# Optimization experiments

Measured on AMD Instinct MI355X. Metric: run time of the kernel, lower is better.

## Reference

```python
import jax, jax.numpy as jnp
import numpy as np

H, W, BS, CIN = 224, 608, 1, 128
CLS = (16, 12, 10)
PAD = (0, 2, 3)
C12 = CLS[0] * CLS[1]            # 192
C123 = C12 * CLS[2]              # 1920
SUPER = 384
CFACT = C123 // SUPER            # 5
PAD_PROJ = 0.1


def _p(key, shape):
    return jax.random.normal(key, shape, dtype=jnp.float32) * 0.05


def setup_inputs() -> dict:
    key = jax.random.key(0)
    ks = iter(jax.random.split(key, 32))
    d = {"x_in": jax.random.normal(next(ks), (BS, CIN, H, W), dtype=jnp.float32)}
    # stage-1: grouped 1x1 convs (groups=height -> one [out,in] matmul per image line)
    for i, (ci, co) in enumerate([(32, 32), (32, 32), (32, CLS[0] + 2 * PAD[0])]):
        d[f"w1_{i}"] = _p(next(ks), (H, co, ci))
        d[f"b1_{i}"] = _p(next(ks), (H, co))
    # stage-2: CondMul tables indexed by line*16 + stage-1 class
    for i, (ci, co) in enumerate([(32, 32), (32, 32), (32, CLS[1] + 2 * PAD[1])]):
        d[f"w2_{i}"] = _p(next(ks), (H * CLS[0], ci, co))
        d[f"b2_{i}"] = _p(next(ks), (H * CLS[0], co))
    # stage-3: CondMul tables indexed by line*192 + stage-12 class
    for i, (ci, co) in enumerate([(32, 32), (32, 32), (32, CLS[2] + 2 * PAD[2])]):
        d[f"w3_{i}"] = _p(next(ks), (H * C12, ci, co))
        d[f"b3_{i}"] = _p(next(ks), (H * C12, co))
    d["wr0"] = _p(next(ks), (H * SUPER, 32, 32))
    d["br0"] = _p(next(ks), (H * SUPER, 32))
    d["wr1"] = _p(next(ks), (H * C123, 32, 1))
    d["br1"] = _p(next(ks), (H * C123, 1))
    return d


def _condmul(x, inds, w, b):
    # CondMul: y[n] = x[n] @ w[inds[n]] + b[inds[n]]
    return jnp.einsum('ni,nio->no', x, w[inds]) + b[inds]


def _forward(x_in, w1, b1, w2, b2, w3, b3, wr0, br0, wr1, br1):
    bs, _, h, w_ = x_in.shape
    lrelu = jax.nn.leaky_relu  # negative_slope=0.01, same as torch default
    offsets = jnp.arange(h, dtype=jnp.int32).reshape(1, 1, h, 1)
    # ---- stage 1: per-line 1x1 grouped conv stack -> argmax class
    x = x_in[:, 0:32].transpose(0, 2, 1, 3)                    # [b,h,32,w]
    for i in range(3):
        x = jnp.einsum('bhiw,hoi->bhow', x, w1[i]) + b1[i][None, :, :, None]
        if i < 2:
            x = lrelu(x)
    x = x.transpose(0, 2, 1, 3)                                 # [b,16,h,w]
    inds1 = jnp.argmax(x, axis=1)[:, None].astype(jnp.int32)    # [b,1,h,w]
    inds1_l = (inds1 + CLS[0] * offsets).reshape(-1)
    # ---- stage 2: CondMul chain conditioned on (line, class1)
    x = x_in[:, 32:64].transpose(0, 2, 3, 1).reshape(-1, 32)    # [N,32]
    for i in range(3):
        x = _condmul(x, inds1_l, w2[i], b2[i])
        if i < 2:
            x = lrelu(x)
    inds2 = jnp.argmax(x, axis=1).astype(jnp.int32).reshape(bs, 1, h, w_)
    inds12 = inds1 * CLS[1] + (inds2 - PAD[1])
    inds12_l = (jnp.clip(inds12, 0, C12 - 1) + C12 * offsets).reshape(-1)
    # ---- stage 3: CondMul chain conditioned on (line, class12)
    x = x_in[:, 64:96].transpose(0, 2, 3, 1).reshape(-1, 32)
    for i in range(3):
        if i < 2:
            x = lrelu(_condmul(x, inds12_l, w3[i], b3[i]))
        else:
            x = _condmul(x, inds12_l, w3[i], b3[i])
    inds3 = jnp.argmax(x, axis=1).astype(jnp.int32).reshape(bs, 1, h, w_)
    inds123 = jnp.clip(inds12 * CLS[2] + (inds3 - PAD[2]), 0, C123 - 1)
    inds = inds123.reshape(-1)
    lines = jnp.broadcast_to(offsets, (bs, 1, h, w_)).reshape(-1)
    inds_l = inds + C123 * lines                                 # per-leaf index
    inds_super_l = inds // CFACT + SUPER * lines                 # superclass index (reg_line_div=1)
    x = x_in[:, 96:128].transpose(0, 2, 3, 1).reshape(-1, 32)
    x = lrelu(_condmul(x, inds_super_l, wr0, br0))
    r = _condmul(x, inds_l, wr1, br1)[:, 0]                      # [N]
    out = (inds.astype(jnp.float32) + r).reshape(bs, 1, h, w_) / float(C123)
    out = (out - PAD_PROJ) / (1.0 - 2.0 * PAD_PROJ)              # undo projector padding
    return out


def reference(x_in, w1_0, b1_0, w1_1, b1_1, w1_2, b1_2,
              w2_0, b2_0, w2_1, b2_1, w2_2, b2_2,
              w3_0, b3_0, w3_1, b3_1, w3_2, b3_2,
              wr0, br0, wr1, br1):
    return _forward(x_in,
                    (w1_0, w1_1, w1_2), (b1_0, b1_1, b1_2),
                    (w2_0, w2_1, w2_2), (b2_0, b2_1, b2_2),
                    (w3_0, w3_1, w3_2), (b3_0, b3_1, b3_2),
                    wr0, br0, wr1, br1)
```

## Files before the change

### kernel.cpp

```cpp
#include <hip/hip_runtime.h>
#include <cstddef>

#define HH 224
#define WW 608
#define HWSZ (HH * WW)

__device__ __forceinline__ float lrelu(float v) { return v > 0.0f ? v : 0.01f * v; }

template <int CO>
__device__ __forceinline__ void cm4(const float* wmat,
                                    const float* bvec,
                                    int s, const float (&act)[8], float (&acc)[CO / 4]) {
    constexpr int CH = CO / 4;
#pragma unroll
    for (int j = 0; j < CH; j++) acc[j] = 0.0f;
#pragma unroll
    for (int sp = 0; sp < 4; sp++) {
#pragma unroll
        for (int ii = 0; ii < 8; ii++) {
            float xi = __shfl(act[ii], sp, 4);
            const float* wr = wmat + (sp * 8 + ii) * CO + s * CH;
            if constexpr (CH == 8) {
                float4 a = *reinterpret_cast<const float4*>(wr);
                float4 b = *reinterpret_cast<const float4*>(wr + 4);
                acc[0] = fmaf(xi, a.x, acc[0]); acc[1] = fmaf(xi, a.y, acc[1]);
                acc[2] = fmaf(xi, a.z, acc[2]); acc[3] = fmaf(xi, a.w, acc[3]);
                acc[4] = fmaf(xi, b.x, acc[4]); acc[5] = fmaf(xi, b.y, acc[5]);
                acc[6] = fmaf(xi, b.z, acc[6]); acc[7] = fmaf(xi, b.w, acc[7]);
            } else {
                float4 a = *reinterpret_cast<const float4*>(wr);
                acc[0] = fmaf(xi, a.x, acc[0]); acc[1] = fmaf(xi, a.y, acc[1]);
                acc[2] = fmaf(xi, a.z, acc[2]); acc[3] = fmaf(xi, a.w, acc[3]);
            }
        }
    }
#pragma unroll
    for (int j = 0; j < CH; j++) acc[j] += bvec[s * CH + j];
}

__device__ __forceinline__ void wb_lrelu8(float (&act)[8], const float (&acc)[8]) {
#pragma unroll
    for (int j = 0; j < 8; j++) act[j] = lrelu(acc[j]);
}

__device__ __forceinline__ int argmax4(const float (&v)[4], int s) {
    float bv = v[0];
    int bi = 4 * s;
#pragma unroll
    for (int j = 1; j < 4; j++) {
        if (v[j] > bv) { bv = v[j]; bi = 4 * s + j; }
    }
#pragma unroll
    for (int m = 1; m <= 2; m <<= 1) {
        float ov = __shfl_xor(bv, m, 4);
        int oi = __shfl_xor(bi, m, 4);
        if (ov > bv || (ov == bv && oi < bi)) { bv = ov; bi = oi; }
    }
    return bi;
}

template <int NF>
__device__ __forceinline__ void stage_mat(float* ws, const float* __restrict__ src, int lane) {
    const float4* s4 = reinterpret_cast<const float4*>(src);
    float4* w4 = reinterpret_cast<float4*>(ws);
#pragma unroll
    for (int t = 0; t < NF / 4 / 64; t++) w4[t * 64 + lane] = s4[t * 64 + lane];
}

extern "C" __global__ __launch_bounds__(256, 4)
void regressor_fused(const float* __restrict__ x_in,
                     const float* __restrict__ w1_0, const float* __restrict__ b1_0,
                     const float* __restrict__ w1_1, const float* __restrict__ b1_1,
                     const float* __restrict__ w1_2, const float* __restrict__ b1_2,
                     const float* __restrict__ w2_0, const float* __restrict__ b2_0,
                     const float* __restrict__ w2_1, const float* __restrict__ b2_1,
                     const float* __restrict__ w2_2, const float* __restrict__ b2_2,
                     const float* __restrict__ w3_0, const float* __restrict__ b3_0,
                     const float* __restrict__ w3_1, const float* __restrict__ b3_1,
                     const float* __restrict__ w3_2, const float* __restrict__ b3_2,
                     const float* __restrict__ wr0, const float* __restrict__ br0,
                     const float* __restrict__ wr1, const float* __restrict__ br1,
                     float* __restrict__ out) {
    const int h = blockIdx.y;
    const int tid = threadIdx.x;
    const int p = tid >> 2;
    const int s = tid & 3;
    const int lane = tid & 63;
    const int w = blockIdx.x * 64 + p;
    const bool valid = (w < WW);
    const int wc = valid ? w : (WW - 1);
    const int base = h * WW + wc;

    __shared__ __align__(16) float sW0[1024];
    __shared__ __align__(16) float sW1[1024];
    __shared__ __align__(16) float sW2[512];
    __shared__ __align__(16) float sUni[4][1024];
    __shared__ __align__(16) float xbuf[32][65];
    __shared__ int skey[64];
    __shared__ int sperm[64];
    __shared__ int sraw[64];
    __shared__ int sraw2[64];
    float* ws = sUni[tid >> 6];

    for (int tt = tid; tt < 1024; tt += 256) {
        int i = tt >> 5, o = tt & 31;
        sW0[tt] = w1_0[h * 1024 + o * 32 + i];
        sW1[tt] = w1_1[h * 1024 + o * 32 + i];
    }
    for (int tt = tid; tt < 512; tt += 256) {
        int i = tt >> 4, o = tt & 15;
        sW2[tt] = w1_2[h * 512 + o * 32 + i];
    }
    __syncthreads();

    float act[8], acc8[8], acc4[4];

#pragma unroll
    for (int ii = 0; ii < 8; ii++) act[ii] = x_in[(8 * s + ii) * HWSZ + base];
    cm4<32>(sW0, b1_0 + h * 32, s, act, acc8);
    wb_lrelu8(act, acc8);
    cm4<32>(sW1, b1_1 + h * 32, s, act, acc8);
    wb_lrelu8(act, acc8);
    cm4<16>(sW2, b1_2 + h * 16, s, act, acc4);
    const int i1 = argmax4(acc4, s);
    if (s == 0) skey[p] = i1;

#pragma unroll
    for (int ii = 0; ii < 8; ii++)
        xbuf[8 * s + ii][p] = x_in[(32 + 8 * s + ii) * HWSZ + base];
    __syncthreads();
    if (tid < 64) {
        int k = skey[tid], rank = 0;
        for (int j = 0; j < 64; j++) {
            int kj = skey[j];
            rank += (kj < k || (kj == k && j < tid)) ? 1 : 0;
        }
        sperm[rank] = tid;
    }
    __syncthreads();

    {
        const int q = sperm[p];
        const int i1q = skey[q];
#pragma unroll
        for (int ii = 0; ii < 8; ii++) act[ii] = xbuf[8 * s + ii][q];
        const int fc = __builtin_amdgcn_readfirstlane(i1q);
        if (__all(i1q == fc)) {
            const size_t u = (size_t)h * 16 + (size_t)fc;
            stage_mat<1024>(ws, w2_0 + u * 1024, lane);
            cm4<32>(ws, b2_0 + u * 32, s, act, acc8);
            wb_lrelu8(act, acc8);
            stage_mat<1024>(ws, w2_1 + u * 1024, lane);
            cm4<32>(ws, b2_1 + u * 32, s, act, acc8);
            wb_lrelu8(act, acc8);
            stage_mat<512>(ws, w2_2 + u * 512, lane);
            cm4<16>(ws, b2_2 + u * 16, s, act, acc4);
        } else {
            const size_t idx2 = (size_t)h * 16 + (size_t)i1q;
            cm4<32>(w2_0 + idx2 * 1024, b2_0 + idx2 * 32, s, act, acc8);
            wb_lrelu8(act, acc8);
            cm4<32>(w2_1 + idx2 * 1024, b2_1 + idx2 * 32, s, act, acc8);
            wb_lrelu8(act, acc8);
            cm4<16>(w2_2 + idx2 * 512, b2_2 + idx2 * 16, s, act, acc4);
        }
        const int i2 = argmax4(acc4, s);
        if (s == 0) sraw[q] = i1q * 12 + (i2 - 2);
    }
    __syncthreads();

#pragma unroll
    for (int ii = 0; ii < 8; ii++)
        xbuf[8 * s + ii][p] = x_in[(64 + 8 * s + ii) * HWSZ + base];
    if (s == 0) skey[p] = min(max(sraw[p], 0), 191);
    __syncthreads();
    if (tid < 64) {
        int k = skey[tid], rank = 0;
        for (int j = 0; j < 64; j++) {
            int kj = skey[j];
            rank += (kj < k || (kj == k && j < tid)) ? 1 : 0;
        }
        sperm[rank] = tid;
    }
    __syncthreads();

    {
        const int q = sperm[p];
        const int r12 = sraw[q];
        const int c12 = min(max(r12, 0), 191);
#pragma unroll
        for (int ii = 0; ii < 8; ii++) act[ii] = xbuf[8 * s + ii][q];
        const int fc = __builtin_amdgcn_readfirstlane(c12);
        if (__all(c12 == fc)) {
            const size_t u = (size_t)h * 192 + (size_t)fc;
            stage_mat<1024>(ws, w3_0 + u * 1024, lane);
            cm4<32>(ws, b3_0 + u * 32, s, act, acc8);
            wb_lrelu8(act, acc8);
            stage_mat<1024>(ws, w3_1 + u * 1024, lane);
            cm4<32>(ws, b3_1 + u * 32, s, act, acc8);
            wb_lrelu8(act, acc8);
            stage_mat<512>(ws, w3_2 + u * 512, lane);
            cm4<16>(ws, b3_2 + u * 16, s, act, acc4);
        } else {
            const size_t idx3 = (size_t)h * 192 + (size_t)c12;
            cm4<32>(w3_0 + idx3 * 1024, b3_0 + idx3 * 32, s, act, acc8);
            wb_lrelu8(act, acc8);
            cm4<32>(w3_1 + idx3 * 1024, b3_1 + idx3 * 32, s, act, acc8);
            wb_lrelu8(act, acc8);
            cm4<16>(w3_2 + idx3 * 512, b3_2 + idx3 * 16, s, act, acc4);
        }
        const int i3 = argmax4(acc4, s);
        if (s == 0) sraw2[q] = min(max(r12 * 10 + (i3 - 3), 0), 1919);
    }
    __syncthreads();

#pragma unroll
    for (int ii = 0; ii < 8; ii++)
        xbuf[8 * s + ii][p] = x_in[(96 + 8 * s + ii) * HWSZ + base];
    if (s == 0) skey[p] = sraw2[p] / 5;
    __syncthreads();
    if (tid < 64) {
        int k = skey[tid], rank = 0;
        for (int j = 0; j < 64; j++) {
            int kj = skey[j];
            rank += (kj < k || (kj == k && j < tid)) ? 1 : 0;
        }
        sperm[rank] = tid;
    }
    __syncthreads();

    {
        const int q = sperm[p];
        const int leaf = sraw2[q];
        const int sup = leaf / 5;
#pragma unroll
        for (int ii = 0; ii < 8; ii++) act[ii] = xbuf[8 * s + ii][q];
        const int fc = __builtin_amdgcn_readfirstlane(sup);
        if (__all(sup == fc)) {
            const size_t u = (size_t)h * 384 + (size_t)fc;
            stage_mat<1024>(ws, wr0 + u * 1024, lane);
            cm4<32>(ws, br0 + u * 32, s, act, acc8);
        } else {
            const size_t idxs = (size_t)h * 384 + (size_t)sup;
            cm4<32>(wr0 + idxs * 1024, br0 + idxs * 32, s, act, acc8);
        }
        wb_lrelu8(act, acc8);

        const size_t idxr = (size_t)h * 1920 + (size_t)leaf;
        const float* wr1r = wr1 + idxr * 32 + 8 * s;
        float4 wa = *reinterpret_cast<const float4*>(wr1r);
        float4 wb = *reinterpret_cast<const float4*>(wr1r + 4);
        float rpart = 0.0f;
        rpart = fmaf(act[0], wa.x, rpart); rpart = fmaf(act[1], wa.y, rpart);
        rpart = fmaf(act[2], wa.z, rpart); rpart = fmaf(act[3], wa.w, rpart);
        rpart = fmaf(act[4], wb.x, rpart); rpart = fmaf(act[5], wb.y, rpart);
        rpart = fmaf(act[6], wb.z, rpart); rpart = fmaf(act[7], wb.w, rpart);
        rpart += __shfl_xor(rpart, 1, 4);
        rpart += __shfl_xor(rpart, 2, 4);
        const float r = rpart + br1[idxr];

        const int wq = blockIdx.x * 64 + q;
        if (s == 0 && wq < WW) {
            float v = ((float)leaf + r) * (1.0f / 1920.0f);
            out[h * WW + wq] = (v - 0.1f) * 1.25f;
        }
    }
}

extern "C" void kernel_launch(void* const* d_in, const int* in_sizes, int n_in,
                              void* d_out, int out_size, void* d_ws, size_t ws_size,
                              hipStream_t stream) {
    const float* p[23];
    for (int i = 0; i < 23; i++) p[i] = (const float*)d_in[i];
    dim3 grid(10, HH);
    regressor_fused<<<grid, 256, 0, stream>>>(
        p[0],
        p[1], p[2], p[3], p[4], p[5], p[6],
        p[7], p[8], p[9], p[10], p[11], p[12],
        p[13], p[14], p[15], p[16], p[17], p[18],
        p[19], p[20], p[21], p[22],
        (float*)d_out);
}
```

Before: 128.7 us.

## Loop over distinct classes per wavefront, staging each weight table in LDS

Each wavefront no longer falls back to per-lane scattered global weight reads when its pixels use different class tables. It now loops over the distinct classes present: it picks the first unfinished lane's class, stages that table into shared memory, runs the whole wavefront through it, and keeps the result only for lanes whose class matches. This trades redundant compute, one pass per distinct class, for coalesced LDS-served weight access. The cost grows with the number of distinct classes per wavefront.

```diff
diff --git a/kernel.cpp b/kernel.cpp
--- a/kernel.cpp
+++ b/kernel.cpp
@@ -8,8 +8,7 @@
 __device__ __forceinline__ float lrelu(float v) { return v > 0.0f ? v : 0.01f * v; }
 
 template <int CO>
-__device__ __forceinline__ void cm4(const float* wmat,
-                                    const float* bvec,
+__device__ __forceinline__ void cm4(const float* wmat, const float* bvec,
                                     int s, const float (&act)[8], float (&acc)[CO / 4]) {
     constexpr int CH = CO / 4;
 #pragma unroll
@@ -87,8 +86,7 @@
     const int s = tid & 3;
     const int lane = tid & 63;
     const int w = blockIdx.x * 64 + p;
-    const bool valid = (w < WW);
-    const int wc = valid ? w : (WW - 1);
+    const int wc = (w < WW) ? w : (WW - 1);
     const int base = h * WW + wc;
 
     __shared__ __align__(16) float sW0[1024];
@@ -113,7 +111,7 @@
     }
     __syncthreads();
 
-    float act[8], acc8[8], acc4[4];
+    float act[8], a0[8], acc8[8], acc4[4];
 
 #pragma unroll
     for (int ii = 0; ii < 8; ii++) act[ii] = x_in[(8 * s + ii) * HWSZ + base];
@@ -130,130 +128,143 @@
         xbuf[8 * s + ii][p] = x_in[(32 + 8 * s + ii) * HWSZ + base];
     __syncthreads();
     if (tid < 64) {
-        int k = skey[tid], rank = 0;
+        int k = skey[tid], r = 0;
         for (int j = 0; j < 64; j++) {
             int kj = skey[j];
-            rank += (kj < k || (kj == k && j < tid)) ? 1 : 0;
-        }
-        sperm[rank] = tid;
+            r += (kj < k || (kj == k && j < tid)) ? 1 : 0;
+        }
+        sperm[r] = tid;
     }
     __syncthreads();
 
     {
         const int q = sperm[p];
-        const int i1q = skey[q];
+        const int mycls = skey[q];
 #pragma unroll
         for (int ii = 0; ii < 8; ii++) act[ii] = xbuf[8 * s + ii][q];
-        const int fc = __builtin_amdgcn_readfirstlane(i1q);
-        if (__all(i1q == fc)) {
-            const size_t u = (size_t)h * 16 + (size_t)fc;
+        bool done = false;
+        for (;;) {
+            unsigned long long m = __ballot(!done);
+            if (!m) break;
+            const int srcl = __ffsll(m) - 1;
+            const int c = __shfl(mycls, srcl);
+            const size_t u = (size_t)h * 16 + (size_t)c;
             stage_mat<1024>(ws, w2_0 + u * 1024, lane);
-            cm4<32>(ws, b2_0 + u * 32, s, act, acc8);
-            wb_lrelu8(act, acc8);
+#pragma unroll
+            for (int ii = 0; ii < 8; ii++) a0[ii] = act[ii];
+            cm4<32>(ws, b2_0 + u * 32, s, a0, acc8);
+            wb_lrelu8(a0, acc8);
             stage_mat<1024>(ws, w2_1 + u * 1024, lane);
-            cm4<32>(ws, b2_1 + u * 32, s, act, acc8);
-            wb_lrelu8(act, acc8);
+            cm4<32>(ws, b2_1 + u * 32, s, a0, acc8);
+            wb_lrelu8(a0, acc8);
             stage_mat<512>(ws, w2_2 + u * 512, lane);
-            cm4<16>(ws, b2_2 + u * 16, s, act, acc4);
-        } else {
-            const size_t idx2 = (size_t)h * 16 + (size_t)i1q;
-            cm4<32>(w2_0 + idx2 * 1024, b2_0 + idx2 * 32, s, act, acc8);
-            wb_lrelu8(act, acc8);
-            cm4<32>(w2_1 + idx2 * 1024, b2_1 + idx2 * 32, s, act, acc8);
-            wb_lrelu8(act, acc8);
-            cm4<16>(w2_2 + idx2 * 512, b2_2 + idx2 * 16, s, act, acc4);
-        }
-        const int i2 = argmax4(acc4, s);
-        if (s == 0) sraw[q] = i1q * 12 + (i2 - 2);
+            cm4<16>(ws, b2_2 + u * 16, s, a0, acc4);
+            const int i2 = argmax4(acc4, s);
+            if (mycls == c) {
+                if (s == 0) sraw[q] = c * 12 + (i2 - 2);
+                done = true;
+            }
+        }
     }
     __syncthreads();
 
 #pragma unroll
     for (int ii = 0; ii < 8; ii++)
         xbuf[8 * s + ii][p] = x_in[(64 + 8 * s + ii) * HWSZ + base];
-    if (s == 0) skey[p] = min(max(sraw[p], 0), 191);
+    if (tid < 64) skey[tid] = min(max(sraw[tid], 0), 191);
     __syncthreads();
     if (tid < 64) {
-        int k = skey[tid], rank = 0;
+        int k = skey[tid], r = 0;
         for (int j = 0; j < 64; j++) {
             int kj = skey[j];
-            rank += (kj < k || (kj == k && j < tid)) ? 1 : 0;
-        }
-        sperm[rank] = tid;
+            r += (kj < k || (kj == k && j < tid)) ? 1 : 0;
+        }
+        sperm[r] = tid;
     }
     __syncthreads();
 
     {
         const int q = sperm[p];
+        const int mycls = skey[q];
         const int r12 = sraw[q];
-        const int c12 = min(max(r12, 0), 191);
 #pragma unroll
         for (int ii = 0; ii < 8; ii++) act[ii] = xbuf[8 * s + ii][q];
-        const int fc = __builtin_amdgcn_readfirstlane(c12);
-        if (__all(c12 == fc)) {
-            const size_t u = (size_t)h * 192 + (size_t)fc;
+        bool done = false;
+        for (;;) {
+            unsigned long long m = __ballot(!done);
+            if (!m) break;
+            const int srcl = __ffsll(m) - 1;
+            const int c = __shfl(mycls, srcl);
+            const size_t u = (size_t)h * 192 + (size_t)c;
             stage_mat<1024>(ws, w3_0 + u * 1024, lane);
-            cm4<32>(ws, b3_0 + u * 32, s, act, acc8);
-            wb_lrelu8(act, acc8);
+#pragma unroll
+            for (int ii = 0; ii < 8; ii++) a0[ii] = act[ii];
+            cm4<32>(ws, b3_0 + u * 32, s, a0, acc8);
+            wb_lrelu8(a0, acc8);
             stage_mat<1024>(ws, w3_1 + u * 1024, lane);
-            cm4<32>(ws, b3_1 + u * 32, s, act, acc8);
-            wb_lrelu8(act, acc8);
+            cm4<32>(ws, b3_1 + u * 32, s, a0, acc8);
+            wb_lrelu8(a0, acc8);
             stage_mat<512>(ws, w3_2 + u * 512, lane);
-            cm4<16>(ws, b3_2 + u * 16, s, act, acc4);
-        } else {
-            const size_t idx3 = (size_t)h * 192 + (size_t)c12;
-            cm4<32>(w3_0 + idx3 * 1024, b3_0 + idx3 * 32, s, act, acc8);
-            wb_lrelu8(act, acc8);
-            cm4<32>(w3_1 + idx3 * 1024, b3_1 + idx3 * 32, s, act, acc8);
-            wb_lrelu8(act, acc8);
-            cm4<16>(w3_2 + idx3 * 512, b3_2 + idx3 * 16, s, act, acc4);
-        }
-        const int i3 = argmax4(acc4, s);
-        if (s == 0) sraw2[q] = min(max(r12 * 10 + (i3 - 3), 0), 1919);
+            cm4<16>(ws, b3_2 + u * 16, s, a0, acc4);
+            const int i3 = argmax4(acc4, s);
+            if (mycls == c) {
+                if (s == 0) sraw2[q] = min(max(r12 * 10 + (i3 - 3), 0), 1919);
+                done = true;
+            }
+        }
     }
     __syncthreads();
 
 #pragma unroll
     for (int ii = 0; ii < 8; ii++)
         xbuf[8 * s + ii][p] = x_in[(96 + 8 * s + ii) * HWSZ + base];
-    if (s == 0) skey[p] = sraw2[p] / 5;
+    if (tid < 64) skey[tid] = sraw2[tid] / 5;
     __syncthreads();
     if (tid < 64) {
-        int k = skey[tid], rank = 0;
+        int k = skey[tid], r = 0;
         for (int j = 0; j < 64; j++) {
             int kj = skey[j];
-            rank += (kj < k || (kj == k && j < tid)) ? 1 : 0;
-        }
-        sperm[rank] = tid;
+            r += (kj < k || (kj == k && j < tid)) ? 1 : 0;
+        }
+        sperm[r] = tid;
     }
     __syncthreads();
 
     {
         const int q = sperm[p];
         const int leaf = sraw2[q];
-        const int sup = leaf / 5;
+        const int sup = skey[q];
 #pragma unroll
         for (int ii = 0; ii < 8; ii++) act[ii] = xbuf[8 * s + ii][q];
-        const int fc = __builtin_amdgcn_readfirstlane(sup);
-        if (__all(sup == fc)) {
-            const size_t u = (size_t)h * 384 + (size_t)fc;
+        float res8[8];
+        bool done = false;
+        for (;;) {
+            unsigned long long m = __ballot(!done);
+            if (!m) break;
+            const int srcl = __ffsll(m) - 1;
+            const int c = __shfl(sup, srcl);
+            const size_t u = (size_t)h * 384 + (size_t)c;
             stage_mat<1024>(ws, wr0 + u * 1024, lane);
-            cm4<32>(ws, br0 + u * 32, s, act, acc8);
-        } else {
-            const size_t idxs = (size_t)h * 384 + (size_t)sup;
-            cm4<32>(wr0 + idxs * 1024, br0 + idxs * 32, s, act, acc8);
-        }
-        wb_lrelu8(act, acc8);
+#pragma unroll
+            for (int ii = 0; ii < 8; ii++) a0[ii] = act[ii];
+            cm4<32>(ws, br0 + u * 32, s, a0, acc8);
+            if (sup == c) {
+#pragma unroll
+                for (int ii = 0; ii < 8; ii++) res8[ii] = acc8[ii];
+                done = true;
+            }
+        }
+        wb_lrelu8(a0, res8);
 
         const size_t idxr = (size_t)h * 1920 + (size_t)leaf;
         const float* wr1r = wr1 + idxr * 32 + 8 * s;
         float4 wa = *reinterpret_cast<const float4*>(wr1r);
         float4 wb = *reinterpret_cast<const float4*>(wr1r + 4);
         float rpart = 0.0f;
-        rpart = fmaf(act[0], wa.x, rpart); rpart = fmaf(act[1], wa.y, rpart);
-        rpart = fmaf(act[2], wa.z, rpart); rpart = fmaf(act[3], wa.w, rpart);
-        rpart = fmaf(act[4], wb.x, rpart); rpart = fmaf(act[5], wb.y, rpart);
-        rpart = fmaf(act[6], wb.z, rpart); rpart = fmaf(act[7], wb.w, rpart);
+        rpart = fmaf(a0[0], wa.x, rpart); rpart = fmaf(a0[1], wa.y, rpart);
+        rpart = fmaf(a0[2], wa.z, rpart); rpart = fmaf(a0[3], wa.w, rpart);
+        rpart = fmaf(a0[4], wb.x, rpart); rpart = fmaf(a0[5], wb.y, rpart);
+        rpart = fmaf(a0[6], wb.z, rpart); rpart = fmaf(a0[7], wb.w, rpart);
         rpart += __shfl_xor(rpart, 1, 4);
         rpart += __shfl_xor(rpart, 2, 4);
         const float r = rpart + br1[idxr];
```

Result: slower. 186.3 us (+44.7%).
